# Kernel tuning notes

Hardware: AMD Instinct MI355X
Metric: run time of the kernel (lower is better)

Reference implementation:

```python
import jax, jax.numpy as jnp
import numpy as np

SCALING = 32.0 / 16.0  # alpha / rank


def _nf4_levels():
    # q_i = Phi^{-1}((i+0.5)/16), normalized to [-1, 1]
    i = jnp.arange(16, dtype=jnp.float32)
    p = jnp.clip((i + 0.5) / 16.0, 1e-6, 1.0 - 1e-6)
    lv = jnp.sqrt(2.0) * jax.scipy.special.erfinv(2.0 * p - 1.0)
    return lv / jnp.max(jnp.abs(lv))


def _dequantize(q_weight, scales):
    # q_weight: (out, in//2) packed nibbles; scales: (out, num_groups)
    out_f, packed = q_weight.shape
    in_f = packed * 2
    hi = (q_weight >> 4) & 15
    lo = q_weight & 15
    idx = jnp.stack([hi, lo], axis=-1).reshape(out_f, in_f)  # interleave hi/lo
    w = _nf4_levels()[idx]  # (out, in)
    num_groups = scales.shape[1]
    block = in_f // num_groups
    w = (w.reshape(out_f, num_groups, block) * scales[:, :, None].astype(jnp.float32))
    return w.reshape(out_f, in_f)


def setup_inputs() -> dict:
    key = jax.random.key(0)
    k1, k2, k3, k4, k5 = jax.random.split(key, 5)
    B, S, IN, OUT, R, BLK = 4, 64, 8192, 8192, 16, 64
    x = jax.random.normal(k1, (B, S, IN), dtype=jnp.float32)
    q_weight = jax.random.randint(k2, (OUT, IN // 2), 0, 256, dtype=jnp.int32)
    scales = jax.random.uniform(k3, (OUT, IN // BLK), dtype=jnp.float32) * 0.02 + 1e-4
    lora_A = jax.random.normal(k4, (R, IN), dtype=jnp.float32) * 0.02
    lora_B = jax.random.normal(k5, (OUT, R), dtype=jnp.float32) * 0.02
    return {"x": x, "q_weight": q_weight, "scales": scales,
            "lora_A": lora_A, "lora_B": lora_B}


def reference(x, q_weight, scales, lora_A, lora_B):
    w = _dequantize(q_weight, scales)               # (out, in) fp32
    base = jnp.einsum('bsi,oi->bso', x, w)          # F.linear(x, W)
    lora = jnp.einsum('bsi,ri->bsr', x, lora_A)     # x @ A^T (dropout p=0)
    lora = jnp.einsum('bsr,or->bso', lora, lora_B)  # @ B^T
    return base + SCALING * lora
```

## Files before the change

kernel.cpp:

```cpp
#include <hip/hip_runtime.h>
#include <hip/hip_bf16.h>
#include <stdint.h>

typedef __attribute__((ext_vector_type(4))) float f32x4;
typedef __attribute__((ext_vector_type(2))) float f32x2;
typedef __attribute__((ext_vector_type(8))) short short8;
typedef __attribute__((ext_vector_type(4))) int int4v;

#define IN_F   8192
#define OUT_F  8192
#define MROWS  256
#define BN     128
#define BK     64
#define NGRP   128

__device__ unsigned short g_xb[MROWS * IN_F];
__device__ float          g_t[MROWS * 16];
__device__ float          g_part[4 * MROWS * OUT_F];

__device__ __constant__ float NF4_LVL[16] = {
  -1.0f,        -0.70756721f, -0.54221982f, -0.41681853f,
  -0.31090474f, -0.21594601f, -0.12734085f, -0.04209530f,
   0.04209530f,  0.12734085f,  0.21594601f,  0.31090474f,
   0.41681853f,  0.54221982f,  0.70756721f,  1.0f };

static __device__ inline uint32_t pkbf(float a, float b) {
  __bf16 ha = (__bf16)a, hb = (__bf16)b;
  return (uint32_t)__builtin_bit_cast(unsigned short, ha)
       | ((uint32_t)__builtin_bit_cast(unsigned short, hb) << 16);
}

__global__ __launch_bounds__(256) void k_convert(const float* __restrict__ x) {
  int cid = blockIdx.x * 256 + threadIdx.x;
  int kt = cid >> 11;
  int r  = (cid >> 3) & 255;
  int c  = cid & 7;
  const float* src = x + (size_t)r * IN_F + kt * 64 + c * 8;
  f32x4 v0 = *(const f32x4*)src;
  f32x4 v1 = *(const f32x4*)(src + 4);
  int4v ov;
  ov[0] = (int)pkbf(v0.x, v0.y); ov[1] = (int)pkbf(v0.z, v0.w);
  ov[2] = (int)pkbf(v1.x, v1.y); ov[3] = (int)pkbf(v1.z, v1.w);
  *(int4v*)(g_xb + (size_t)kt * 16384 + r * 64 + ((c ^ (r & 7)) << 3)) = ov;
}

__global__ __launch_bounds__(256) void k_xa(const float* __restrict__ x,
                                            const float* __restrict__ lora_A) {
  int m = blockIdx.x, tid = threadIdx.x;
  float acc[16];
#pragma unroll
  for (int r = 0; r < 16; ++r) acc[r] = 0.f;
  const float* xr = x + (size_t)m * IN_F;
  for (int it = 0; it < 8; ++it) {
    int k = (tid + it * 256) * 4;
    f32x4 xv = *(const f32x4*)(xr + k);
#pragma unroll
    for (int r = 0; r < 16; ++r) {
      f32x4 av = *(const f32x4*)(lora_A + (size_t)r * IN_F + k);
      acc[r] += xv.x * av.x + xv.y * av.y + xv.z * av.z + xv.w * av.w;
    }
  }
#pragma unroll
  for (int r = 0; r < 16; ++r) {
    float v = acc[r];
#pragma unroll
    for (int off = 32; off; off >>= 1) v += __shfl_xor(v, off, 64);
    acc[r] = v;
  }
  __shared__ float sm[4][16];
  int lane = tid & 63, wave = tid >> 6;
  if (lane == 0) {
#pragma unroll
    for (int r = 0; r < 16; ++r) sm[wave][r] = acc[r];
  }
  __syncthreads();
  if (tid < 16)
    g_t[m * 16 + tid] = 2.0f * (sm[0][tid] + sm[1][tid] + sm[2][tid] + sm[3][tid]);
}

__global__ __launch_bounds__(256) void k_lora(const float* __restrict__ lora_B,
                                              float* __restrict__ out) {
  int bid = blockIdx.x;
  int m = bid >> 5;
  int n = ((bid & 31) << 8) + threadIdx.x;
  const float* tr = g_t + m * 16;
  f32x4 t0 = *(const f32x4*)tr,       t1 = *(const f32x4*)(tr + 4);
  f32x4 t2 = *(const f32x4*)(tr + 8), t3 = *(const f32x4*)(tr + 12);
  const float* br = lora_B + (size_t)n * 16;
  f32x4 b0 = *(const f32x4*)br,       b1 = *(const f32x4*)(br + 4);
  f32x4 b2 = *(const f32x4*)(br + 8), b3 = *(const f32x4*)(br + 12);
  float v = t0.x*b0.x + t0.y*b0.y + t0.z*b0.z + t0.w*b0.w
          + t1.x*b1.x + t1.y*b1.y + t1.z*b1.z + t1.w*b1.w
          + t2.x*b2.x + t2.y*b2.y + t2.z*b2.z + t2.w*b2.w
          + t3.x*b3.x + t3.y*b3.y + t3.z*b3.z + t3.w*b3.w;
  out[(size_t)m * OUT_F + n] = v;
}

__global__ __launch_bounds__(512, 2) void k_gemm(
    const int* __restrict__ qw, const float* __restrict__ scales)
{
  __shared__ unsigned short Al[MROWS * BK];
  __shared__ unsigned short Bl[BN * BK];
  __shared__ f32x2 lut[256];

  int tid = threadIdx.x;
  int lane = tid & 63, wave = tid >> 6;

  if (tid < 256) {
    f32x2 e; e.x = NF4_LVL[tid >> 4]; e.y = NF4_LVL[tid & 15];
    lut[tid] = e;
  }

  int flat = blockIdx.y * 64 + blockIdx.x;
  int wg = (flat & 7) * 32 + (flat >> 3);
  int bx = wg & 63, bz = wg >> 6;

  int n0 = bx * BN;
  int ktg0 = bz * 32;

  f32x4 acc[4][4];
#pragma unroll
  for (int i = 0; i < 4; ++i)
#pragma unroll
    for (int j = 0; j < 4; ++j) acc[i][j] = (f32x4){0.f, 0.f, 0.f, 0.f};

  int wr = wave >> 1, wc = wave & 1;
  int wm = wr * 64, wn = wc * 64;

  __syncthreads();

  for (int kt = 0; kt < 32; ++kt) {
    int ktg = ktg0 + kt;
    if (kt) __syncthreads();

    {
      const char* src = (const char*)g_xb + (size_t)ktg * 32768 + tid * 16;
      char* dst = (char*)Al + tid * 16;
#pragma unroll
      for (int j = 0; j < 4; ++j) {
        __builtin_amdgcn_global_load_lds(
            (const __attribute__((address_space(1))) void*)(src + j * 8192),
            (__attribute__((address_space(3))) void*)(dst + j * 8192), 16, 0, 0);
      }
    }

#pragma unroll
    for (int t2 = 0; t2 < 2; ++t2) {
      int u = tid + t2 * 512;
      int n = u >> 3, c = u & 7;
      int grow = n0 + n;
      float s = scales[(size_t)grow * NGRP + ktg];
      int4v q = *(const int4v*)(qw + (size_t)grow * (IN_F / 2) + ktg * 32 + c * 4);
      int4v ov;
#pragma unroll
      for (int e = 0; e < 4; ++e) {
        f32x2 lv = lut[q[e] & 255];
        ov[e] = (int)pkbf(lv.x * s, lv.y * s);
      }
      *(int4v*)((char*)Bl + n * 128 + ((c ^ (n & 7)) << 4)) = ov;
    }
    __syncthreads();

#pragma unroll
    for (int kk = 0; kk < 2; ++kk) {
      short8 af[4], bfv[4];
#pragma unroll
      for (int mi = 0; mi < 4; ++mi) {
        int r = wm + mi * 16 + (lane & 15);
        int cch = (kk * 4 + (lane >> 4)) ^ (r & 7);
        af[mi] = *(const short8*)((const char*)Al + r * 128 + cch * 16);
      }
#pragma unroll
      for (int ni = 0; ni < 4; ++ni) {
        int n = wn + ni * 16 + (lane & 15);
        int cch = (kk * 4 + (lane >> 4)) ^ (n & 7);
        bfv[ni] = *(const short8*)((const char*)Bl + n * 128 + cch * 16);
      }
#pragma unroll
      for (int mi = 0; mi < 4; ++mi)
#pragma unroll
        for (int ni = 0; ni < 4; ++ni)
          acc[mi][ni] = __builtin_amdgcn_mfma_f32_16x16x32_bf16(
              af[mi], bfv[ni], acc[mi][ni], 0, 0, 0);
    }
  }

  float* op = g_part + (size_t)bz * MROWS * OUT_F;
#pragma unroll
  for (int mi = 0; mi < 4; ++mi) {
#pragma unroll
    for (int ni = 0; ni < 4; ++ni) {
      int m = wm + mi * 16 + (lane >> 4) * 4;
      int nn = n0 + wn + ni * 16 + (lane & 15);
#pragma unroll
      for (int j = 0; j < 4; ++j)
        op[(size_t)(m + j) * OUT_F + nn] = acc[mi][ni][j];
    }
  }
}

__global__ __launch_bounds__(256) void k_reduce(float* __restrict__ out) {
  size_t i = ((size_t)blockIdx.x * 256 + threadIdx.x) * 4;
  f32x4 v = *(f32x4*)(out + i);
#pragma unroll
  for (int s = 0; s < 4; ++s)
    v += *(const f32x4*)(g_part + (size_t)s * MROWS * OUT_F + i);
  *(f32x4*)(out + i) = v;
}

extern "C" void kernel_launch(void* const* d_in, const int* in_sizes, int n_in,
                              void* d_out, int out_size, void* d_ws, size_t ws_size,
                              hipStream_t stream) {
  const float* x  = (const float*)d_in[0];
  const int*   qw = (const int*)d_in[1];
  const float* sc = (const float*)d_in[2];
  const float* lA = (const float*)d_in[3];
  const float* lB = (const float*)d_in[4];
  float* out = (float*)d_out;

  k_convert<<<1024, 256, 0, stream>>>(x);
  k_xa<<<256, 256, 0, stream>>>(x, lA);
  k_lora<<<8192, 256, 0, stream>>>(lB, out);
  k_gemm<<<dim3(64, 4), 512, 0, stream>>>(qw, sc);
  k_reduce<<<2048, 256, 0, stream>>>(out);
}
```

Before: 112.1 us.

## Double-buffer GEMM LDS tiles with register prefetch and fuse LoRA into reduce

```diff
diff --git a/kernel.cpp b/kernel.cpp
--- a/kernel.cpp
+++ b/kernel.cpp
@@ -3,7 +3,6 @@
 #include <stdint.h>
 
 typedef __attribute__((ext_vector_type(4))) float f32x4;
-typedef __attribute__((ext_vector_type(2))) float f32x2;
 typedef __attribute__((ext_vector_type(8))) short short8;
 typedef __attribute__((ext_vector_type(4))) int int4v;
 
@@ -78,133 +77,162 @@
     g_t[m * 16 + tid] = 2.0f * (sm[0][tid] + sm[1][tid] + sm[2][tid] + sm[3][tid]);
 }
 
-__global__ __launch_bounds__(256) void k_lora(const float* __restrict__ lora_B,
-                                              float* __restrict__ out) {
-  int bid = blockIdx.x;
-  int m = bid >> 5;
-  int n = ((bid & 31) << 8) + threadIdx.x;
+__global__ __launch_bounds__(512, 2) void k_gemm(
+    const int* __restrict__ qw, const float* __restrict__ scales)
+{
+  __shared__ unsigned short Al[2][MROWS * BK];
+  __shared__ unsigned short Bl[2][BN * BK];
+  __shared__ float lut16[16];
+
+  int tid = threadIdx.x;
+  int lane = tid & 63, wave = tid >> 6;
+  if (tid < 16) lut16[tid] = NF4_LVL[tid];
+  __syncthreads();
+
+  int flat = blockIdx.y * 64 + blockIdx.x;
+  int wg = (flat & 7) * 32 + (flat >> 3);
+  int bx = wg & 63, bz = wg >> 6;
+  int n0 = bx * BN;
+  int ktg0 = bz * 32;
+
+  int n_0 = tid >> 3, c_0 = tid & 7;
+  int n_1 = n_0 + 64;
+  const int* qr0 = qw + (size_t)(n0 + n_0) * (IN_F / 2) + c_0 * 4;
+  const int* qr1 = qw + (size_t)(n0 + n_1) * (IN_F / 2) + c_0 * 4;
+  const float* sr0 = scales + (size_t)(n0 + n_0) * NGRP;
+  const float* sr1 = scales + (size_t)(n0 + n_1) * NGRP;
+  int boff0 = n_0 * 128 + ((c_0 ^ (n_0 & 7)) << 4);
+  int boff1 = boff0 + 64 * 128;
+
+  f32x4 acc[4][4];
+#pragma unroll
+  for (int i = 0; i < 4; ++i)
+#pragma unroll
+    for (int j = 0; j < 4; ++j) acc[i][j] = (f32x4){0.f, 0.f, 0.f, 0.f};
+
+  int wr = wave >> 1, wc = wave & 1;
+  int wm = wr * 64, wn = wc * 64;
+
+  auto stageA = [&](int buf, int kt) {
+    const char* src = (const char*)g_xb + (size_t)kt * 32768 + tid * 16;
+    char* dst = (char*)(&Al[buf][0]) + tid * 16;
+#pragma unroll
+    for (int j = 0; j < 4; ++j)
+      __builtin_amdgcn_global_load_lds(
+          (const __attribute__((address_space(1))) void*)(src + j * 8192),
+          (__attribute__((address_space(3))) void*)(dst + j * 8192), 16, 0, 0);
+  };
+
+  auto dqst = [&](int buf, int4v q0, float s0, int4v q1, float s1) {
+    char* Bb = (char*)(&Bl[buf][0]);
+    int4v ov;
+#pragma unroll
+    for (int e = 0; e < 4; ++e) {
+      float hi = lut16[(q0[e] >> 4) & 15];
+      float lo = lut16[q0[e] & 15];
+      ov[e] = (int)pkbf(hi * s0, lo * s0);
+    }
+    *(int4v*)(Bb + boff0) = ov;
+#pragma unroll
+    for (int e = 0; e < 4; ++e) {
+      float hi = lut16[(q1[e] >> 4) & 15];
+      float lo = lut16[q1[e] & 15];
+      ov[e] = (int)pkbf(hi * s1, lo * s1);
+    }
+    *(int4v*)(Bb + boff1) = ov;
+  };
+
+  auto compute = [&](int buf) {
+    const char* Ab = (const char*)(&Al[buf][0]);
+    const char* Bb = (const char*)(&Bl[buf][0]);
+#pragma unroll
+    for (int kk = 0; kk < 2; ++kk) {
+      short8 af[4], bfv[4];
+#pragma unroll
+      for (int mi = 0; mi < 4; ++mi) {
+        int r = wm + mi * 16 + (lane & 15);
+        int cch = (kk * 4 + (lane >> 4)) ^ (r & 7);
+        af[mi] = *(const short8*)(Ab + r * 128 + cch * 16);
+      }
+#pragma unroll
+      for (int ni = 0; ni < 4; ++ni) {
+        int n = wn + ni * 16 + (lane & 15);
+        int cch = (kk * 4 + (lane >> 4)) ^ (n & 7);
+        bfv[ni] = *(const short8*)(Bb + n * 128 + cch * 16);
+      }
+      __builtin_amdgcn_s_setprio(1);
+#pragma unroll
+      for (int mi = 0; mi < 4; ++mi)
+#pragma unroll
+        for (int ni = 0; ni < 4; ++ni)
+          acc[mi][ni] = __builtin_amdgcn_mfma_f32_16x16x32_bf16(
+              af[mi], bfv[ni], acc[mi][ni], 0, 0, 0);
+      __builtin_amdgcn_s_setprio(0);
+    }
+  };
+
+  int4v qa0 = *(const int4v*)(qr0 + ktg0 * 32);
+  int4v qa1 = *(const int4v*)(qr1 + ktg0 * 32);
+  float sa0 = sr0[ktg0], sa1 = sr1[ktg0];
+  stageA(0, ktg0);
+  int4v qb0 = *(const int4v*)(qr0 + (ktg0 + 1) * 32);
+  int4v qb1 = *(const int4v*)(qr1 + (ktg0 + 1) * 32);
+  float sb0 = sr0[ktg0 + 1], sb1 = sr1[ktg0 + 1];
+  dqst(0, qa0, sa0, qa1, sa1);
+  asm volatile("s_waitcnt vmcnt(0) lgkmcnt(0)" ::: "memory");
+  __builtin_amdgcn_s_barrier();
+
+  for (int t = 0; t < 31; ++t) {
+    int c = t & 1;
+    int kn = ktg0 + ((t < 30) ? (t + 2) : 0);
+    int4v qn0 = *(const int4v*)(qr0 + kn * 32);
+    int4v qn1 = *(const int4v*)(qr1 + kn * 32);
+    float sn0 = sr0[kn], sn1 = sr1[kn];
+    stageA(c ^ 1, ktg0 + t + 1);
+    dqst(c ^ 1, qb0, sb0, qb1, sb1);
+    compute(c);
+    asm volatile("s_waitcnt vmcnt(0) lgkmcnt(0)" ::: "memory");
+    __builtin_amdgcn_s_barrier();
+    qb0 = qn0; qb1 = qn1; sb0 = sn0; sb1 = sn1;
+  }
+  compute(1);
+
+  float* op = g_part + (size_t)bz * MROWS * OUT_F;
+#pragma unroll
+  for (int mi = 0; mi < 4; ++mi) {
+#pragma unroll
+    for (int ni = 0; ni < 4; ++ni) {
+      int m = wm + mi * 16 + (lane >> 4) * 4;
+      int nn = n0 + wn + ni * 16 + (lane & 15);
+#pragma unroll
+      for (int j = 0; j < 4; ++j)
+        op[(size_t)(m + j) * OUT_F + nn] = acc[mi][ni][j];
+    }
+  }
+}
+
+__global__ __launch_bounds__(256) void k_reduce(const float* __restrict__ lora_B,
+                                                float* __restrict__ out) {
+  size_t i = ((size_t)blockIdx.x * 256 + threadIdx.x) * 4;
+  int m = (int)(i >> 13);
+  int n = (int)(i & 8191);
+  f32x4 v = *(const f32x4*)(g_part + i);
+  v += *(const f32x4*)(g_part + (size_t)1 * MROWS * OUT_F + i);
+  v += *(const f32x4*)(g_part + (size_t)2 * MROWS * OUT_F + i);
+  v += *(const f32x4*)(g_part + (size_t)3 * MROWS * OUT_F + i);
   const float* tr = g_t + m * 16;
   f32x4 t0 = *(const f32x4*)tr,       t1 = *(const f32x4*)(tr + 4);
   f32x4 t2 = *(const f32x4*)(tr + 8), t3 = *(const f32x4*)(tr + 12);
-  const float* br = lora_B + (size_t)n * 16;
-  f32x4 b0 = *(const f32x4*)br,       b1 = *(const f32x4*)(br + 4);
-  f32x4 b2 = *(const f32x4*)(br + 8), b3 = *(const f32x4*)(br + 12);
-  float v = t0.x*b0.x + t0.y*b0.y + t0.z*b0.z + t0.w*b0.w
+#pragma unroll
+  for (int j = 0; j < 4; ++j) {
+    const float* br = lora_B + (size_t)(n + j) * 16;
+    f32x4 b0 = *(const f32x4*)br,       b1 = *(const f32x4*)(br + 4);
+    f32x4 b2 = *(const f32x4*)(br + 8), b3 = *(const f32x4*)(br + 12);
+    v[j] += t0.x*b0.x + t0.y*b0.y + t0.z*b0.z + t0.w*b0.w
           + t1.x*b1.x + t1.y*b1.y + t1.z*b1.z + t1.w*b1.w
           + t2.x*b2.x + t2.y*b2.y + t2.z*b2.z + t2.w*b2.w
           + t3.x*b3.x + t3.y*b3.y + t3.z*b3.z + t3.w*b3.w;
-  out[(size_t)m * OUT_F + n] = v;
-}
-
-__global__ __launch_bounds__(512, 2) void k_gemm(
-    const int* __restrict__ qw, const float* __restrict__ scales)
-{
-  __shared__ unsigned short Al[MROWS * BK];
-  __shared__ unsigned short Bl[BN * BK];
-  __shared__ f32x2 lut[256];
-
-  int tid = threadIdx.x;
-  int lane = tid & 63, wave = tid >> 6;
-
-  if (tid < 256) {
-    f32x2 e; e.x = NF4_LVL[tid >> 4]; e.y = NF4_LVL[tid & 15];
-    lut[tid] = e;
-  }
-
-  int flat = blockIdx.y * 64 + blockIdx.x;
-  int wg = (flat & 7) * 32 + (flat >> 3);
-  int bx = wg & 63, bz = wg >> 6;
-
-  int n0 = bx * BN;
-  int ktg0 = bz * 32;
-
-  f32x4 acc[4][4];
-#pragma unroll
-  for (int i = 0; i < 4; ++i)
-#pragma unroll
-    for (int j = 0; j < 4; ++j) acc[i][j] = (f32x4){0.f, 0.f, 0.f, 0.f};
-
-  int wr = wave >> 1, wc = wave & 1;
-  int wm = wr * 64, wn = wc * 64;
-
-  __syncthreads();
-
-  for (int kt = 0; kt < 32; ++kt) {
-    int ktg = ktg0 + kt;
-    if (kt) __syncthreads();
-
-    {
-      const char* src = (const char*)g_xb + (size_t)ktg * 32768 + tid * 16;
-      char* dst = (char*)Al + tid * 16;
-#pragma unroll
-      for (int j = 0; j < 4; ++j) {
-        __builtin_amdgcn_global_load_lds(
-            (const __attribute__((address_space(1))) void*)(src + j * 8192),
-            (__attribute__((address_space(3))) void*)(dst + j * 8192), 16, 0, 0);
-      }
-    }
-
-#pragma unroll
-    for (int t2 = 0; t2 < 2; ++t2) {
-      int u = tid + t2 * 512;
-      int n = u >> 3, c = u & 7;
-      int grow = n0 + n;
-      float s = scales[(size_t)grow * NGRP + ktg];
-      int4v q = *(const int4v*)(qw + (size_t)grow * (IN_F / 2) + ktg * 32 + c * 4);
-      int4v ov;
-#pragma unroll
-      for (int e = 0; e < 4; ++e) {
-        f32x2 lv = lut[q[e] & 255];
-        ov[e] = (int)pkbf(lv.x * s, lv.y * s);
-      }
-      *(int4v*)((char*)Bl + n * 128 + ((c ^ (n & 7)) << 4)) = ov;
-    }
-    __syncthreads();
-
-#pragma unroll
-    for (int kk = 0; kk < 2; ++kk) {
-      short8 af[4], bfv[4];
-#pragma unroll
-      for (int mi = 0; mi < 4; ++mi) {
-        int r = wm + mi * 16 + (lane & 15);
-        int cch = (kk * 4 + (lane >> 4)) ^ (r & 7);
-        af[mi] = *(const short8*)((const char*)Al + r * 128 + cch * 16);
-      }
-#pragma unroll
-      for (int ni = 0; ni < 4; ++ni) {
-        int n = wn + ni * 16 + (lane & 15);
-        int cch = (kk * 4 + (lane >> 4)) ^ (n & 7);
-        bfv[ni] = *(const short8*)((const char*)Bl + n * 128 + cch * 16);
-      }
-#pragma unroll
-      for (int mi = 0; mi < 4; ++mi)
-#pragma unroll
-        for (int ni = 0; ni < 4; ++ni)
-          acc[mi][ni] = __builtin_amdgcn_mfma_f32_16x16x32_bf16(
-              af[mi], bfv[ni], acc[mi][ni], 0, 0, 0);
-    }
-  }
-
-  float* op = g_part + (size_t)bz * MROWS * OUT_F;
-#pragma unroll
-  for (int mi = 0; mi < 4; ++mi) {
-#pragma unroll
-    for (int ni = 0; ni < 4; ++ni) {
-      int m = wm + mi * 16 + (lane >> 4) * 4;
-      int nn = n0 + wn + ni * 16 + (lane & 15);
-#pragma unroll
-      for (int j = 0; j < 4; ++j)
-        op[(size_t)(m + j) * OUT_F + nn] = acc[mi][ni][j];
-    }
-  }
-}
-
-__global__ __launch_bounds__(256) void k_reduce(float* __restrict__ out) {
-  size_t i = ((size_t)blockIdx.x * 256 + threadIdx.x) * 4;
-  f32x4 v = *(f32x4*)(out + i);
-#pragma unroll
-  for (int s = 0; s < 4; ++s)
-    v += *(const f32x4*)(g_part + (size_t)s * MROWS * OUT_F + i);
+  }
   *(f32x4*)(out + i) = v;
 }
 
@@ -220,7 +248,6 @@
 
   k_convert<<<1024, 256, 0, stream>>>(x);
   k_xa<<<256, 256, 0, stream>>>(x, lA);
-  k_lora<<<8192, 256, 0, stream>>>(lB, out);
   k_gemm<<<dim3(64, 4), 512, 0, stream>>>(qw, sc);
-  k_reduce<<<2048, 256, 0, stream>>>(out);
-}
+  k_reduce<<<2048, 256, 0, stream>>>(lB, out);
+}
```

Result: faster. 107.5 us (-4.1%).
